# Optimization experiments

Hardware: AMD Instinct MI355X
Metric: run time of the kernel (lower is better)

The kernel has to match this reference:

```python
import jax, jax.numpy as jnp
import numpy as np

E, TOP, C, H, W, B = 8, 2, 128, 96, 96, 8
NUM_GATES = 4
KH = 3  # capsule conv kernel


def setup_inputs() -> dict:
    key = jax.random.key(0)
    ks = jax.random.split(key, 6)
    x = jax.random.normal(ks[0], (B, C, H, W), jnp.float32)
    # xavier_uniform for gates: bound = sqrt(6/(fan_in+fan_out))
    bound = float(np.sqrt(6.0 / (C + E)))
    G = jax.random.uniform(ks[1], (NUM_GATES, C, E), jnp.float32, -bound, bound)
    # per-expert capsule convs: the 16 parallel (C->capsule_dim) 3x3 convs are
    # stacked along the output-channel axis into one (C->C) conv per expert
    Wc = jax.random.normal(ks[2], (E, C, C, KH, KH), jnp.float32) * (1.0 / np.sqrt(C * KH * KH))
    bc = jax.random.normal(ks[3], (E, C), jnp.float32) * 0.01
    # 1x1 output projection per expert
    Wp = jax.random.normal(ks[4], (E, C, C), jnp.float32) * (1.0 / np.sqrt(C))
    bp = jax.random.normal(ks[5], (E, C), jnp.float32) * 0.01
    return {"x": x, "G": G, "Wc": Wc, "bc": bc, "Wp": Wp, "bp": bp}


def _squash(u):
    # squash over the full channel dim (dim=1), matching the torch module
    sn = jnp.sum(u * u, axis=1, keepdims=True)
    return (sn / (1.0 + sn)) * u / jnp.sqrt(sn + 1e-8)


def _expert(x, wc, bc, wp, bp):
    u = jax.lax.conv_general_dilated(
        x, wc, window_strides=(1, 1), padding='SAME',
        dimension_numbers=('NCHW', 'OIHW', 'NCHW')) + bc[None, :, None, None]
    u = jax.nn.relu(u)
    u = _squash(u)
    return jnp.einsum('bchw,oc->bohw', u, wp) + bp[None, :, None, None]


def _cv_squared(v):
    v = v.astype(jnp.float32)
    return jnp.var(v, ddof=1) / (jnp.mean(v) ** 2 + 1e-10)


def reference(x, G, Wc, bc, Wp, bp):
    Bn = x.shape[0]
    # run every expert on the full batch (dense equivalent of the masked dispatch)
    y_all = jax.vmap(lambda wc_, bc_, wp_, bp_: _expert(x, wc_, bc_, wp_, bp_))(
        Wc, bc, Wp, bp)  # [E, B, C, H, W]
    x_gap = jnp.mean(x, axis=(2, 3))  # [B, C]  (adaptive avg pool to 1x1)
    ys, losses = [], []
    for g in range(NUM_GATES):
        probs = jax.nn.softmax(x_gap @ G[g], axis=1)           # [B, E]
        tv, ti = jax.lax.top_k(probs, TOP)                     # [B, TOP]
        tw = jax.nn.softmax(tv, axis=1)                        # renormalized top-k weights
        out = jnp.zeros_like(x)
        for k in range(TOP):
            y_sel = y_all[ti[:, k], jnp.arange(Bn)]            # gather per-sample expert out
            out = out + y_sel * tw[:, k][:, None, None, None]
        ys.append(out)
        losses.append(_cv_squared(jnp.sum(probs, axis=0)))     # cv^2 of expert usage
    total_loss = jnp.mean(jnp.stack(losses))
    return (*ys, total_loss)
```

## Files before the change

kernel.cpp:

```cpp
#include <hip/hip_runtime.h>
#include <math.h>

#define CHW 9216
#define OPG 9437184

typedef unsigned short u16;
typedef __attribute__((ext_vector_type(8))) short short8;
typedef __attribute__((ext_vector_type(4))) float f32x4;

#define WS_XT  8192
#define WS_AT  18882560
#define WS_WPT 21241856

__device__ __forceinline__ u16 f2bf(float f) {
    unsigned u = __float_as_uint(f);
    u += 0x7fff + ((u >> 16) & 1);
    return (u16)(u >> 16);
}

__device__ __forceinline__ void gload_lds16(const void* g, void* l) {
    __builtin_amdgcn_global_load_lds(
        (const __attribute__((address_space(1))) void*)g,
        (__attribute__((address_space(3))) void*)l, 16, 0, 0);
}

__global__ void gap_kernel(const float* __restrict__ x, float* __restrict__ xgap) {
    int bc = blockIdx.x;
    const float* p = x + (size_t)bc * CHW;
    float s = 0.f;
    for (int i = threadIdx.x; i < CHW; i += 256) s += p[i];
    __shared__ float red[256];
    red[threadIdx.x] = s;
    __syncthreads();
    for (int off = 128; off > 0; off >>= 1) {
        if (threadIdx.x < off) red[threadIdx.x] += red[threadIdx.x + off];
        __syncthreads();
    }
    if (threadIdx.x == 0) xgap[bc] = red[0] * (1.0f / 9216.0f);
}

__global__ void gate_kernel(const float* __restrict__ G, float* __restrict__ ws,
                            float* __restrict__ loss_out) {
    __shared__ float gap_s[1024];
    __shared__ float logits[64];
    __shared__ float probs[64];
    __shared__ float vsum[8];
    __shared__ float losses[4];
    int t = threadIdx.x;
    for (int i = t; i < 1024; i += 64) gap_s[i] = ws[i];
    int b = t >> 3, e = t & 7;
    int* iw = (int*)(ws + 1344);
    float* wt = ws + 1408;
    __syncthreads();
    for (int g = 0; g < 4; ++g) {
        float acc = 0.f;
        const float* Gg = G + g * 1024;
        for (int c = 0; c < 128; ++c) acc += gap_s[b * 128 + c] * Gg[c * 8 + e];
        logits[t] = acc;
        __syncthreads();
        float m = -1e30f;
        for (int j = 0; j < 8; ++j) m = fmaxf(m, logits[b * 8 + j]);
        float den = 0.f;
        for (int j = 0; j < 8; ++j) den += expf(logits[b * 8 + j] - m);
        float pr = expf(acc - m) / den;
        probs[t] = pr;
        __syncthreads();
        if (e == 0) {
            int i0 = 0; float v0 = probs[b * 8];
            for (int j = 1; j < 8; ++j) { float v = probs[b * 8 + j]; if (v > v0) { v0 = v; i0 = j; } }
            int i1 = -1; float v1 = -1e30f;
            for (int j = 0; j < 8; ++j) { if (j == i0) continue; float v = probs[b * 8 + j]; if (v > v1) { v1 = v; i1 = j; } }
            float r = expf(v1 - v0);
            float inv = 1.f / (1.f + r);
            iw[g * 16 + b * 2 + 0] = i0;
            iw[g * 16 + b * 2 + 1] = i1;
            wt[g * 16 + b * 2 + 0] = inv;
            wt[g * 16 + b * 2 + 1] = r * inv;
        }
        if (t < 8) {
            float v = 0.f;
            for (int bb = 0; bb < 8; ++bb) v += probs[bb * 8 + t];
            vsum[t] = v;
        }
        __syncthreads();
        if (t == 0) {
            float mean = 0.f;
            for (int j = 0; j < 8; ++j) mean += vsum[j];
            mean *= 0.125f;
            float var = 0.f;
            for (int j = 0; j < 8; ++j) { float d = vsum[j] - mean; var += d * d; }
            var *= (1.f / 7.f);
            losses[g] = var / (mean * mean + 1e-10f);
        }
        __syncthreads();
    }
    if (t == 0) loss_out[0] = 0.25f * (losses[0] + losses[1] + losses[2] + losses[3]);
}

__global__ void pre_x(const float* __restrict__ x, u16* __restrict__ Xt) {
    int h = blockIdx.x, b = blockIdx.y, t = threadIdx.x;
    __shared__ u16 lds[12288];
    const float* xb = x + ((size_t)b * 128) * CHW + h * 96;
    for (int i = t; i < 12288; i += 256) {
        int c = i / 96, w = i - c * 96;
        lds[(c >> 6) * 6144 + w * 64 + ((c & 63) ^ ((w & 7) << 3))] = f2bf(xb[(size_t)c * CHW + w]);
    }
    __syncthreads();
    const unsigned* l32 = (const unsigned*)lds;
    unsigned* o32 = (unsigned*)Xt;
    for (int i = t; i < 6144; i += 256) {
        int hf = (i >= 3072) ? 1 : 0;
        int rem = i - hf * 3072;
        o32[((size_t)(b * 2 + hf) * 96 + h) * 3072 + rem] = l32[i];
    }
}

__global__ void pre_wc2(const float* __restrict__ Wc, u16* __restrict__ At2) {
    int idx = blockIdx.x * 256 + threadIdx.x;
    int s = idx & 7;
    int lane = (idx >> 3) & 63;
    int mb = (idx >> 9) & 3;
    int mi = (idx >> 11) & 1;
    int ck = (idx >> 12) & 1;
    int rem = idx >> 13;
    int r = rem % 9;
    int rem2 = rem / 9;
    int hf = rem2 & 1;
    int e = rem2 >> 1;
    int l15 = lane & 15, quad = lane >> 4;
    int o = mi * 64 + mb * 16 + l15;
    int cin = hf * 64 + ck * 32 + quad * 8 + s;
    size_t src = (((size_t)e * 128 + o) * 128 + cin) * 9 + r;
    At2[idx] = f2bf(Wc[src]);
}

__global__ void pre_wp(const float* __restrict__ Wp, u16* __restrict__ Wpt) {
    int i = blockIdx.x * 256 + threadIdx.x;
    if (i < 131072) Wpt[i] = f2bf(Wp[i]);
}

__launch_bounds__(512, 2)
__global__ void expert_kernel(const u16* __restrict__ Xt, const u16* __restrict__ At2,
                              const u16* __restrict__ Wpt,
                              const float* __restrict__ bc, const float* __restrict__ bp,
                              const float* __restrict__ ws, float* __restrict__ out) {
    int hs = blockIdx.x, b = blockIdx.y, g = blockIdx.z;
    int h0 = hs * 2;
    int t = threadIdx.x, lane = t & 63, wv = t >> 6;
    int mi = wv & 1, ni = wv >> 1;
    int l15 = lane & 15, quad = lane >> 4, q8 = quad * 8;
    int nrow = ni >> 1;
    int ncb = (ni & 1) * 48;

    const int* iw = (const int*)(ws + 1344);
    const float* wt = ws + 1408;
    int ee[2];
    float wwt[2];
    ee[0] = iw[g * 16 + b * 2 + 0]; ee[1] = iw[g * 16 + b * 2 + 1];
    wwt[0] = wt[g * 16 + b * 2 + 0]; wwt[1] = wt[g * 16 + b * 2 + 1];

    __shared__ __align__(16) char smem[58368];
    u16* Hs = (u16*)smem;
    float* part_s = (float*)smem;
    u16* v_s = (u16*)(smem + 9216);

    f32x4 zero = {0.f, 0.f, 0.f, 0.f};
    f32x4 acc[2][12];
    #pragma unroll
    for (int i = 0; i < 12; ++i) { acc[0][i] = zero; acc[1][i] = zero; }

    int abase = mi * 2048 + lane * 8;

    for (int hf = 0; hf < 2; ++hf) {
        __syncthreads();
        const u16* Xb = Xt + (size_t)(b * 2 + hf) * 96 * 6144;
        for (int rr = 0; rr < 4; ++rr) {
            int row = h0 - 1 + rr;
            u16* dst = Hs + rr * 6272;
            if (row >= 0 && row < 96) {
                const u16* src = Xb + (size_t)row * 6144;
                for (int i = t; i < 768; i += 512)
                    gload_lds16(src + i * 8, dst + 64 + i * 8);
            } else {
                uint4 z; z.x = z.y = z.z = z.w = 0u;
                for (int i = t; i < 784; i += 512) *(uint4*)(dst + i * 8) = z;
            }
        }
        if (t < 64) {
            uint4 z; z.x = z.y = z.z = z.w = 0u;
            int rr = t >> 4, cs = (t >> 3) & 1, p = t & 7;
            *(uint4*)(Hs + rr * 6272 + cs * 97 * 64 + p * 8) = z;
        }
        __syncthreads();

        const u16* A0 = At2 + (size_t)(ee[0] * 2 + hf) * 73728;
        const u16* A1 = At2 + (size_t)(ee[1] * 2 + hf) * 73728;
        short8 c0[4], c1[4];
        #pragma unroll
        for (int mb = 0; mb < 4; ++mb) {
            c0[mb] = *(const short8*)(A0 + abase + mb * 512);
            c1[mb] = *(const short8*)(A1 + abase + mb * 512);
        }
        #pragma unroll
        for (int s = 0; s < 18; ++s) {
            int r = s >> 1, ck = s & 1;
            int dyi = (r * 11) >> 5;
            int dxi = r - dyi * 3;
            int hb = (nrow + dyi) * 12544;
            int sn = (s < 17) ? s + 1 : 17;
            int noff = sn * 4096 + abase;
            short8 n0[4], n1[4];
            #pragma unroll
            for (int mb = 0; mb < 4; ++mb) {
                n0[mb] = *(const short8*)(A0 + noff + mb * 512);
                n1[mb] = *(const short8*)(A1 + noff + mb * 512);
            }
            short8 bv[3];
            #pragma unroll
            for (int j = 0; j < 3; ++j) {
                int col = ncb + j * 16 + l15 + dxi;
                int ba = hb + col * 128 + ((q8 ^ (((col - 1) & 7) << 3)) << 1);
                bv[j] = *(const short8*)(smem + (ba ^ (ck << 6)));
            }
            #pragma unroll
            for (int mb = 0; mb < 4; ++mb)
                #pragma unroll
                for (int j = 0; j < 3; ++j) {
                    acc[0][mb * 3 + j] = __builtin_amdgcn_mfma_f32_16x16x32_bf16(c0[mb], bv[j], acc[0][mb * 3 + j], 0, 0, 0);
                    acc[1][mb * 3 + j] = __builtin_amdgcn_mfma_f32_16x16x32_bf16(c1[mb], bv[j], acc[1][mb * 3 + j], 0, 0, 0);
                }
            #pragma unroll
            for (int mb = 0; mb < 4; ++mb) { c0[mb] = n0[mb]; c1[mb] = n1[mb]; }
        }
    }

    #pragma unroll
    for (int xp = 0; xp < 2; ++xp) {
        int e_ = ee[xp];
        __syncthreads();
        #pragma unroll
        for (int j = 0; j < 3; ++j) {
            int n = ni * 48 + j * 16 + l15;
            float ssum = 0.f;
            #pragma unroll
            for (int mb = 0; mb < 4; ++mb) {
                f32x4 a = acc[xp][mb * 3 + j];
                #pragma unroll
                for (int rg = 0; rg < 4; ++rg) {
                    float u = fmaxf(a[rg] + bc[e_ * 128 + mi * 64 + mb * 16 + quad * 4 + rg], 0.f);
                    a[rg] = u; ssum += u * u;
                }
                acc[xp][mb * 3 + j] = a;
            }
            part_s[n * 12 + mi * 4 + quad] = ssum;
        }
        __syncthreads();
        #pragma unroll
        for (int j = 0; j < 3; ++j) {
            int n = ni * 48 + j * 16 + l15;
            f32x4 p0 = *(const f32x4*)(part_s + n * 12);
            f32x4 p1 = *(const f32x4*)(part_s + n * 12 + 4);
            float sn2 = p0[0] + p0[1] + p0[2] + p0[3] + p1[0] + p1[1] + p1[2] + p1[3];
            float fsj = sn2 / ((1.f + sn2) * sqrtf(sn2 + 1e-8f));
            int sw = (n & 7) << 3;
            #pragma unroll
            for (int mb = 0; mb < 4; ++mb) {
                f32x4 a = acc[xp][mb * 3 + j];
                short4 pk;
                pk.x = (short)f2bf(a[0] * fsj); pk.y = (short)f2bf(a[1] * fsj);
                pk.z = (short)f2bf(a[2] * fsj); pk.w = (short)f2bf(a[3] * fsj);
                int cb = mb * 16 + quad * 4;
                *(short4*)(v_s + n * 128 + ((cb ^ sw) | (mi << 6))) = pk;
            }
        }
        __syncthreads();
        #pragma unroll
        for (int i = 0; i < 12; ++i) acc[xp][i] = zero;
        const u16* We_ = Wpt + (size_t)e_ * 16384;
        #pragma unroll
        for (int kk = 0; kk < 4; ++kk) {
            short8 af[4];
            #pragma unroll
            for (int mb = 0; mb < 4; ++mb)
                af[mb] = *(const short8*)(We_ + (mi * 64 + mb * 16 + l15) * 128 + kk * 32 + q8);
            short8 bvv[3];
            #pragma unroll
            for (int j = 0; j < 3; ++j) {
                int n = ni * 48 + j * 16 + l15;
                int sw = (n & 7) << 3;
                int pos = ((kk & 2) << 5) | ((((kk & 1) << 5) + q8) ^ sw);
                bvv[j] = *(const short8*)(v_s + n * 128 + pos);
            }
            #pragma unroll
            for (int mb = 0; mb < 4; ++mb)
                #pragma unroll
                for (int j = 0; j < 3; ++j)
                    acc[xp][mb * 3 + j] = __builtin_amdgcn_mfma_f32_16x16x32_bf16(af[mb], bvv[j], acc[xp][mb * 3 + j], 0, 0, 0);
        }
    }

    int row = h0 + nrow;
    #pragma unroll
    for (int mb = 0; mb < 4; ++mb)
        #pragma unroll
        for (int rg = 0; rg < 4; ++rg) {
            int o = mi * 64 + mb * 16 + quad * 4 + rg;
            float y0b = bp[ee[0] * 128 + o];
            float y1b = bp[ee[1] * 128 + o];
            size_t obase = (size_t)g * OPG + ((size_t)(b * 128 + o)) * CHW + (size_t)row * 96;
            #pragma unroll
            for (int j = 0; j < 3; ++j) {
                float y0 = acc[0][mb * 3 + j][rg] + y0b;
                float y1 = acc[1][mb * 3 + j][rg] + y1b;
                out[obase + ncb + j * 16 + l15] = wwt[0] * y0 + wwt[1] * y1;
            }
        }
}

extern "C" void kernel_launch(void* const* d_in, const int* in_sizes, int n_in,
                              void* d_out, int out_size, void* d_ws, size_t ws_size,
                              hipStream_t stream) {
    const float* x  = (const float*)d_in[0];
    const float* G  = (const float*)d_in[1];
    const float* Wc = (const float*)d_in[2];
    const float* bc = (const float*)d_in[3];
    const float* Wp = (const float*)d_in[4];
    const float* bp = (const float*)d_in[5];
    float* out = (float*)d_out;
    float* ws  = (float*)d_ws;
    u16* Xt  = (u16*)((char*)d_ws + WS_XT);
    u16* At2 = (u16*)((char*)d_ws + WS_AT);
    u16* Wpt = (u16*)((char*)d_ws + WS_WPT);

    gap_kernel<<<dim3(1024), dim3(256), 0, stream>>>(x, ws);
    gate_kernel<<<dim3(1), dim3(64), 0, stream>>>(G, ws, out + (size_t)4 * OPG);
    pre_x<<<dim3(96, 8), dim3(256), 0, stream>>>(x, Xt);
    pre_wc2<<<dim3(4608), dim3(256), 0, stream>>>(Wc, At2);
    pre_wp<<<dim3(512), dim3(256), 0, stream>>>(Wp, Wpt);
    expert_kernel<<<dim3(48, 8, 4), dim3(512), 0, stream>>>(Xt, At2, Wpt, bc, bp, ws, out);
}
```

Baseline: 451.0 us.

## Stage both input halves in LDS at once and deepen register prefetch

LDS grows to hold both halves of the input-channel halo tiles, so a single barrier covers both halves and the barrier between them is gone. Weight fragments are now prefetched two steps ahead from global memory, and the LDS B-operand reads are double-buffered one step ahead. This is meant to hide global and LDS latency behind the MFMA work. In exchange, about 100KB of LDS per block and more live registers may lower occupancy.

```diff
diff --git a/kernel.cpp b/kernel.cpp
--- a/kernel.cpp
+++ b/kernel.cpp
@@ -159,8 +159,7 @@
     ee[0] = iw[g * 16 + b * 2 + 0]; ee[1] = iw[g * 16 + b * 2 + 1];
     wwt[0] = wt[g * 16 + b * 2 + 0]; wwt[1] = wt[g * 16 + b * 2 + 1];
 
-    __shared__ __align__(16) char smem[58368];
-    u16* Hs = (u16*)smem;
+    __shared__ __align__(16) char smem[100352];
     float* part_s = (float*)smem;
     u16* v_s = (u16*)(smem + 9216);
 
@@ -171,12 +170,13 @@
 
     int abase = mi * 2048 + lane * 8;
 
+    #pragma unroll
     for (int hf = 0; hf < 2; ++hf) {
-        __syncthreads();
         const u16* Xb = Xt + (size_t)(b * 2 + hf) * 96 * 6144;
+        u16* Hb = (u16*)(smem + hf * 50176);
         for (int rr = 0; rr < 4; ++rr) {
             int row = h0 - 1 + rr;
-            u16* dst = Hs + rr * 6272;
+            u16* dst = Hb + rr * 6272;
             if (row >= 0 && row < 96) {
                 const u16* src = Xb + (size_t)row * 6144;
                 for (int i = t; i < 768; i += 512)
@@ -189,48 +189,65 @@
         if (t < 64) {
             uint4 z; z.x = z.y = z.z = z.w = 0u;
             int rr = t >> 4, cs = (t >> 3) & 1, p = t & 7;
-            *(uint4*)(Hs + rr * 6272 + cs * 97 * 64 + p * 8) = z;
-        }
-        __syncthreads();
-
+            *(uint4*)(Hb + rr * 6272 + cs * 97 * 64 + p * 8) = z;
+        }
+    }
+    __syncthreads();
+
+    #pragma unroll
+    for (int hf = 0; hf < 2; ++hf) {
+        const char* Hb = smem + hf * 50176;
         const u16* A0 = At2 + (size_t)(ee[0] * 2 + hf) * 73728;
         const u16* A1 = At2 + (size_t)(ee[1] * 2 + hf) * 73728;
-        short8 c0[4], c1[4];
-        #pragma unroll
-        for (int mb = 0; mb < 4; ++mb) {
-            c0[mb] = *(const short8*)(A0 + abase + mb * 512);
-            c1[mb] = *(const short8*)(A1 + abase + mb * 512);
-        }
+
+        short8 cf[2][2][4];
+        #pragma unroll
+        for (int p = 0; p < 2; ++p)
+            #pragma unroll
+            for (int mb = 0; mb < 4; ++mb) {
+                cf[p][0][mb] = *(const short8*)(A0 + p * 4096 + abase + mb * 512);
+                cf[p][1][mb] = *(const short8*)(A1 + p * 4096 + abase + mb * 512);
+            }
+
+        short8 bv[2][3];
+        #pragma unroll
+        for (int j = 0; j < 3; ++j) {
+            int col = ncb + j * 16 + l15;
+            int ba = nrow * 12544 + col * 128 + ((q8 ^ (((col - 1) & 7) << 3)) << 1);
+            bv[0][j] = *(const short8*)(Hb + ba);
+        }
+
         #pragma unroll
         for (int s = 0; s < 18; ++s) {
-            int r = s >> 1, ck = s & 1;
-            int dyi = (r * 11) >> 5;
-            int dxi = r - dyi * 3;
-            int hb = (nrow + dyi) * 12544;
-            int sn = (s < 17) ? s + 1 : 17;
-            int noff = sn * 4096 + abase;
-            short8 n0[4], n1[4];
-            #pragma unroll
-            for (int mb = 0; mb < 4; ++mb) {
-                n0[mb] = *(const short8*)(A0 + noff + mb * 512);
-                n1[mb] = *(const short8*)(A1 + noff + mb * 512);
-            }
-            short8 bv[3];
-            #pragma unroll
-            for (int j = 0; j < 3; ++j) {
-                int col = ncb + j * 16 + l15 + dxi;
-                int ba = hb + col * 128 + ((q8 ^ (((col - 1) & 7) << 3)) << 1);
-                bv[j] = *(const short8*)(smem + (ba ^ (ck << 6)));
+            const int sl = s & 1, nsl = sl ^ 1;
+            if (s < 17) {
+                int s1 = s + 1;
+                int r1 = s1 >> 1, ck1 = s1 & 1;
+                int dyi1 = (r1 * 11) >> 5;
+                int dxi1 = r1 - dyi1 * 3;
+                int hb1 = (nrow + dyi1) * 12544;
+                #pragma unroll
+                for (int j = 0; j < 3; ++j) {
+                    int col = ncb + j * 16 + l15 + dxi1;
+                    int ba = hb1 + col * 128 + ((q8 ^ (((col - 1) & 7) << 3)) << 1);
+                    bv[nsl][j] = *(const short8*)(Hb + (ba ^ (ck1 << 6)));
+                }
             }
             #pragma unroll
             for (int mb = 0; mb < 4; ++mb)
                 #pragma unroll
                 for (int j = 0; j < 3; ++j) {
-                    acc[0][mb * 3 + j] = __builtin_amdgcn_mfma_f32_16x16x32_bf16(c0[mb], bv[j], acc[0][mb * 3 + j], 0, 0, 0);
-                    acc[1][mb * 3 + j] = __builtin_amdgcn_mfma_f32_16x16x32_bf16(c1[mb], bv[j], acc[1][mb * 3 + j], 0, 0, 0);
+                    acc[0][mb * 3 + j] = __builtin_amdgcn_mfma_f32_16x16x32_bf16(cf[sl][0][mb], bv[sl][j], acc[0][mb * 3 + j], 0, 0, 0);
+                    acc[1][mb * 3 + j] = __builtin_amdgcn_mfma_f32_16x16x32_bf16(cf[sl][1][mb], bv[sl][j], acc[1][mb * 3 + j], 0, 0, 0);
                 }
-            #pragma unroll
-            for (int mb = 0; mb < 4; ++mb) { c0[mb] = n0[mb]; c1[mb] = n1[mb]; }
+            if (s < 16) {
+                int noff = (s + 2) * 4096 + abase;
+                #pragma unroll
+                for (int mb = 0; mb < 4; ++mb) {
+                    cf[sl][0][mb] = *(const short8*)(A0 + noff + mb * 512);
+                    cf[sl][1][mb] = *(const short8*)(A1 + noff + mb * 512);
+                }
+            }
         }
     }
 
```

Result: no change. 448.7 us (-0.5%).

## Stage conv weights through LDS with a 4-deep async pipeline across both channel halves

Applied to the files above, without the earlier changes.

Conv weight fragments for the two selected experts are no longer loaded from global memory straight into registers. They are staged into a 4-slot LDS ring with async global-to-LDS loads, issued two steps ahead and guarded by explicit vmcnt waits and barriers. The two channel-half loops become one 36-step loop, and the second half's input rows are prefetched mid-loop. MFMA sections are raised in priority with s_setprio. LDS usage roughly doubles, which can cut occupancy, and the manual waitcnt accounting is fragile.

```diff
diff --git a/kernel.cpp b/kernel.cpp
--- a/kernel.cpp
+++ b/kernel.cpp
@@ -159,7 +159,7 @@
     ee[0] = iw[g * 16 + b * 2 + 0]; ee[1] = iw[g * 16 + b * 2 + 1];
     wwt[0] = wt[g * 16 + b * 2 + 0]; wwt[1] = wt[g * 16 + b * 2 + 1];
 
-    __shared__ __align__(16) char smem[58368];
+    __shared__ __align__(16) char smem[115712];
     u16* Hs = (u16*)smem;
     float* part_s = (float*)smem;
     u16* v_s = (u16*)(smem + 9216);
@@ -169,70 +169,91 @@
     #pragma unroll
     for (int i = 0; i < 12; ++i) { acc[0][i] = zero; acc[1][i] = zero; }
 
-    int abase = mi * 2048 + lane * 8;
-
-    for (int hf = 0; hf < 2; ++hf) {
-        __syncthreads();
-        const u16* Xb = Xt + (size_t)(b * 2 + hf) * 96 * 6144;
+    const u16* Ab0 = At2 + (size_t)(ee[0] * 2) * 73728;
+    const u16* Ab1 = At2 + (size_t)(ee[1] * 2) * 73728;
+
+    #define ASRC(P, U) ((P) + ((U) >= 18 ? 73728 + ((U) - 18) * 4096 : (U) * 4096))
+    #define STAGE(U) { u16* ab_ = (u16*)(smem + 50176 + ((U) & 3) * 16384);          \
+                       gload_lds16(ASRC(Ab0, (U)) + t * 8, ab_ + t * 8);             \
+                       gload_lds16(ASRC(Ab1, (U)) + t * 8, ab_ + 4096 + t * 8); }
+
+    {
+        uint4 z; z.x = z.y = z.z = z.w = 0u;
+        #pragma unroll
         for (int rr = 0; rr < 4; ++rr) {
             int row = h0 - 1 + rr;
-            u16* dst = Hs + rr * 6272;
+            if (row < 0 || row >= 96)
+                for (int i = t; i < 784; i += 512) *(uint4*)(Hs + rr * 6272 + i * 8) = z;
+        }
+        if (t < 64) {
+            int rr = t >> 4, cs = (t >> 3) & 1, p = t & 7;
+            *(uint4*)(Hs + rr * 6272 + cs * 97 * 64 + p * 8) = z;
+        }
+        const u16* Xb = Xt + (size_t)(b * 2 + 0) * 96 * 6144;
+        #pragma unroll
+        for (int rr = 0; rr < 4; ++rr) {
+            int row = h0 - 1 + rr;
             if (row >= 0 && row < 96) {
                 const u16* src = Xb + (size_t)row * 6144;
-                for (int i = t; i < 768; i += 512)
-                    gload_lds16(src + i * 8, dst + 64 + i * 8);
-            } else {
-                uint4 z; z.x = z.y = z.z = z.w = 0u;
-                for (int i = t; i < 784; i += 512) *(uint4*)(dst + i * 8) = z;
-            }
-        }
-        if (t < 64) {
-            uint4 z; z.x = z.y = z.z = z.w = 0u;
-            int rr = t >> 4, cs = (t >> 3) & 1, p = t & 7;
-            *(uint4*)(Hs + rr * 6272 + cs * 97 * 64 + p * 8) = z;
-        }
-        __syncthreads();
-
-        const u16* A0 = At2 + (size_t)(ee[0] * 2 + hf) * 73728;
-        const u16* A1 = At2 + (size_t)(ee[1] * 2 + hf) * 73728;
-        short8 c0[4], c1[4];
+                u16* dst = Hs + rr * 6272 + 64;
+                for (int i = t; i < 768; i += 512) gload_lds16(src + i * 8, dst + i * 8);
+            }
+        }
+    }
+    STAGE(0); STAGE(1);
+    __syncthreads();
+
+    #pragma unroll
+    for (int u = 0; u < 36; ++u) {
+        if (u == 18) {
+            __builtin_amdgcn_s_barrier();
+            const u16* Xb = Xt + (size_t)(b * 2 + 1) * 96 * 6144;
+            #pragma unroll
+            for (int rr = 0; rr < 4; ++rr) {
+                int row = h0 - 1 + rr;
+                if (row >= 0 && row < 96) {
+                    const u16* src = Xb + (size_t)row * 6144;
+                    u16* dst = Hs + rr * 6272 + 64;
+                    for (int i = t; i < 768; i += 512) gload_lds16(src + i * 8, dst + i * 8);
+                }
+            }
+        }
+        if (u <= 33) STAGE(u + 2);
+        if (u == 18 || u == 35) asm volatile("s_waitcnt vmcnt(0)" ::: "memory");
+        else if (u == 34)       asm volatile("s_waitcnt vmcnt(2)" ::: "memory");
+        else                    asm volatile("s_waitcnt vmcnt(4)" ::: "memory");
+        __builtin_amdgcn_s_barrier();
+
+        int s = (u >= 18) ? u - 18 : u;
+        int r = s >> 1, ck = s & 1;
+        int dyi = r / 3, dxi = r - dyi * 3;
+        const u16* ab = (const u16*)(smem + 50176 + (u & 3) * 16384);
+
+        short8 af0[4], af1[4], bv[3];
         #pragma unroll
         for (int mb = 0; mb < 4; ++mb) {
-            c0[mb] = *(const short8*)(A0 + abase + mb * 512);
-            c1[mb] = *(const short8*)(A1 + abase + mb * 512);
-        }
-        #pragma unroll
-        for (int s = 0; s < 18; ++s) {
-            int r = s >> 1, ck = s & 1;
-            int dyi = (r * 11) >> 5;
-            int dxi = r - dyi * 3;
-            int hb = (nrow + dyi) * 12544;
-            int sn = (s < 17) ? s + 1 : 17;
-            int noff = sn * 4096 + abase;
-            short8 n0[4], n1[4];
-            #pragma unroll
-            for (int mb = 0; mb < 4; ++mb) {
-                n0[mb] = *(const short8*)(A0 + noff + mb * 512);
-                n1[mb] = *(const short8*)(A1 + noff + mb * 512);
-            }
-            short8 bv[3];
+            af0[mb] = *(const short8*)(ab + mi * 2048 + mb * 512 + lane * 8);
+            af1[mb] = *(const short8*)(ab + 4096 + mi * 2048 + mb * 512 + lane * 8);
+        }
+        int hb = (nrow + dyi) * 12544;
+        #pragma unroll
+        for (int j = 0; j < 3; ++j) {
+            int col = ncb + j * 16 + l15 + dxi;
+            int ba = hb + col * 128 + ((q8 ^ (((col - 1) & 7) << 3)) << 1);
+            bv[j] = *(const short8*)(smem + (ba ^ (ck << 6)));
+        }
+        __builtin_amdgcn_s_setprio(1);
+        #pragma unroll
+        for (int mb = 0; mb < 4; ++mb)
             #pragma unroll
             for (int j = 0; j < 3; ++j) {
-                int col = ncb + j * 16 + l15 + dxi;
-                int ba = hb + col * 128 + ((q8 ^ (((col - 1) & 7) << 3)) << 1);
-                bv[j] = *(const short8*)(smem + (ba ^ (ck << 6)));
-            }
-            #pragma unroll
-            for (int mb = 0; mb < 4; ++mb)
-                #pragma unroll
-                for (int j = 0; j < 3; ++j) {
-                    acc[0][mb * 3 + j] = __builtin_amdgcn_mfma_f32_16x16x32_bf16(c0[mb], bv[j], acc[0][mb * 3 + j], 0, 0, 0);
-                    acc[1][mb * 3 + j] = __builtin_amdgcn_mfma_f32_16x16x32_bf16(c1[mb], bv[j], acc[1][mb * 3 + j], 0, 0, 0);
-                }
-            #pragma unroll
-            for (int mb = 0; mb < 4; ++mb) { c0[mb] = n0[mb]; c1[mb] = n1[mb]; }
-        }
-    }
+                acc[0][mb * 3 + j] = __builtin_amdgcn_mfma_f32_16x16x32_bf16(af0[mb], bv[j], acc[0][mb * 3 + j], 0, 0, 0);
+                acc[1][mb * 3 + j] = __builtin_amdgcn_mfma_f32_16x16x32_bf16(af1[mb], bv[j], acc[1][mb * 3 + j], 0, 0, 0);
+            }
+        __builtin_amdgcn_s_setprio(0);
+    }
+    #undef STAGE
+    #undef ASRC
 
     #pragma unroll
     for (int xp = 0; xp < 2; ++xp) {
```

Result: faster. 429.7 us (-4.7%).
